# Performance work log

Measured on AMD Instinct MI355X. Metric: run time of the kernel, lower is better.

The kernel has to match this reference:

```python
import jax, jax.numpy as jnp
import numpy as np

D_STATE = 512
D_MODEL = 512
BATCH = 8
SEQ = 4096
DT_MIN, DT_MAX = 1e-3, 0.1
LN_EPS = 1e-5


def setup_inputs() -> dict:
    key = jax.random.key(0)
    ks = jax.random.split(key, 4)
    x = jax.random.normal(ks[0], (BATCH, SEQ, D_MODEL), dtype=jnp.float32)
    volatility_scale = jax.random.uniform(ks[1], (BATCH, SEQ, 1), dtype=jnp.float32)
    # parameters (mirroring the torch module's __init__)
    log_lambda_real = jnp.linspace(np.log(DT_MIN), np.log(DT_MAX), D_STATE).astype(jnp.float32)
    log_b = jax.random.uniform(ks[2], (D_STATE, 1), dtype=jnp.float32, minval=-0.5, maxval=0.5)
    c = jax.random.normal(ks[3], (1, D_STATE), dtype=jnp.float32) / np.sqrt(D_STATE)
    log_d = jnp.zeros((1,), jnp.float32)
    ts = np.array([1.0 / 24.0, 1.0, 5.0, 21.0, 63.0], np.float32)
    extra = np.linspace(63.0, 189.0, D_STATE - len(ts), dtype=np.float32)
    log_step = jnp.log(jnp.asarray(np.concatenate([ts, extra])))
    volatility_gate = jnp.ones((D_MODEL,), jnp.float32)
    alpha = jnp.asarray(0.7, jnp.float32)
    ln_weight = jnp.ones((D_STATE,), jnp.float32)
    ln_bias = jnp.zeros((D_STATE,), jnp.float32)
    return dict(x=x, volatility_scale=volatility_scale,
                log_lambda_real=log_lambda_real, log_b=log_b, c=c, log_d=log_d,
                log_step=log_step, volatility_gate=volatility_gate, alpha=alpha,
                ln_weight=ln_weight, ln_bias=ln_bias)


def reference(x, volatility_scale, log_lambda_real, log_b, c, log_d,
              log_step, volatility_gate, alpha, ln_weight, ln_bias):
    lam = -jnp.exp(log_lambda_real)              # [N], negative real poles
    step = jnp.exp(log_step)                     # [N], per-state timescale
    b = jnp.exp(log_b)[:, 0]                     # [N]
    d = jnp.exp(log_d)                           # [1], skip gain
    # bilinear (Tustin) discretization, paired per state
    z = step * lam                               # [N]
    a_disc = (2.0 + z) / (2.0 - z)               # [N]
    b_disc = step * (1.0 + a_disc) * b / 2.0     # [N]
    gate = jax.nn.sigmoid(volatility_gate)       # [D]
    c_vec = c[0]                                 # [N]

    def layer_norm(h):
        mu = jnp.mean(h, axis=-1, keepdims=True)
        var = jnp.var(h, axis=-1, keepdims=True)
        return (h - mu) * jax.lax.rsqrt(var + LN_EPS) * ln_weight + ln_bias

    def scan_step(h, inp):
        x_t, v_t = inp                           # [B,D], [B,1]
        h = a_disc * h + b_disc * x_t            # diagonal SSM update, [B,N]
        h = layer_norm(h)
        h = h / (1.0 + gate * v_t)               # volatility gating
        y_t = jnp.sum(h * c_vec, axis=-1, keepdims=True) + d * x_t  # [B,D]
        return h, y_t

    h0 = jnp.zeros((x.shape[0], a_disc.shape[0]), x.dtype)
    xs = (jnp.swapaxes(x, 0, 1), jnp.swapaxes(volatility_scale, 0, 1))  # time-major
    _, ys = jax.lax.scan(scan_step, h0, xs)      # [S,B,D]
    y = jnp.swapaxes(ys, 0, 1)                   # [B,S,D]
    al = jax.nn.sigmoid(alpha)
    return al * x + (1.0 - al) * y
```

## Files before the change

kernel.cpp:

```cpp
#include <hip/hip_runtime.h>
#include <cstdint>
#include <cstddef>

#define BATCH 8
#define SEQ   4096
#define DS    512
#define JPL   8
#define BLK   8
#define NBLK  (SEQ / BLK)

typedef float v2f __attribute__((ext_vector_type(2)));
typedef float v4f __attribute__((ext_vector_type(4)));

static __device__ __forceinline__ v2f lo2(v4f x) { return __builtin_shufflevector(x, x, 0, 1); }
static __device__ __forceinline__ v2f hi2(v4f x) { return __builtin_shufflevector(x, x, 2, 3); }

template <int CTRL>
__device__ __forceinline__ float dpp_add(float v) {
  int t = __builtin_amdgcn_update_dpp(0, __builtin_bit_cast(int, v), CTRL, 0xF, 0xF, true);
  return v + __builtin_bit_cast(float, t);
}
__device__ __forceinline__ float wave_sum64(float v) {
  v = dpp_add<0x111>(v);
  v = dpp_add<0x112>(v);
  v = dpp_add<0x114>(v);
  v = dpp_add<0x118>(v);
  v = dpp_add<0x142>(v);
  v = dpp_add<0x143>(v);
  return v;
}
__device__ __forceinline__ float bcast63(float v) {
  return __builtin_bit_cast(float, __builtin_amdgcn_readlane(__builtin_bit_cast(int, v), 63));
}

__device__ __forceinline__ void ld16(const float* g, float* l) {
  __builtin_amdgcn_global_load_lds(
      (const __attribute__((address_space(1))) void*)g,
      (__attribute__((address_space(3))) void*)l, 16, 0, 0);
}

__global__ __launch_bounds__(192, 1) void ssm_scan(
    const float* __restrict__ x, const float* __restrict__ vol,
    const float* __restrict__ llr, const float* __restrict__ logb,
    const float* __restrict__ cvec, const float* __restrict__ lstp,
    const float* __restrict__ vgat, const float* __restrict__ lnw,
    const float* __restrict__ lnb, float* __restrict__ sp)
{
  __shared__ float X0[4096], X1[4096];
  __shared__ float R0[4096], R1[4096];
  __shared__ float SC0[512], SC1[512];

  const int b    = blockIdx.x;
  const int lane = threadIdx.x & 63;
  const int wid  = threadIdx.x >> 6;

  if (wid == 1) {
    const float* xg = x + (size_t)b * SEQ * DS + lane * JPL;
    float* spb = sp + (size_t)b * SEQ;

    auto dma_blk = [&](int blk, float* Xs) {
#pragma unroll
      for (int u = 0; u < BLK; ++u) {
        const float* row = xg + (size_t)(blk * BLK + u) * DS;
        ld16(row,     Xs + u * 512);
        ld16(row + 4, Xs + u * 512 + 256);
      }
    };
    auto red_copy = [&](const float* SCs, int blk) {
      float s[BLK];
#pragma unroll
      for (int u = 0; u < BLK; ++u) s[u] = wave_sum64(SCs[u * 64 + lane]);
      if (lane == 63) {
#pragma unroll
        for (int u = 0; u < BLK; ++u) spb[blk * BLK + u] = s[u];
      }
    };

    dma_blk(0, X0);
    __syncthreads();
#pragma unroll 1
    for (int i2 = 0; i2 < NBLK; i2 += 2) {
      dma_blk(i2 + 1, X1);
      if (i2 > 0) red_copy(SC1, i2 - 1);
      __syncthreads();
      if (i2 + 2 < NBLK) dma_blk(i2 + 2, X0);
      red_copy(SC0, i2);
      __syncthreads();
    }
    red_copy(SC1, NBLK - 1);
  } else if (wid == 2) {
    v2f gate[4];
#pragma unroll
    for (int j = 0; j < JPL; ++j)
      gate[j >> 1][j & 1] = 1.0f / (1.0f + expf(-vgat[lane * JPL + j]));
    const float* vg = vol + (size_t)b * SEQ;

    auto rg_blk = [&](v4f Va, v4f Vb, float* Rs) {
#pragma unroll
      for (int u = 0; u < BLK; ++u) {
        float vt = (u < 4) ? Va[u] : Vb[u - 4];
        v4f r0, r1;
#pragma unroll
        for (int k = 0; k < 4; ++k) {
          v2f den = gate[k] * vt + 1.0f;
          float q0 = __builtin_amdgcn_rcpf(den.x);
          float q1 = __builtin_amdgcn_rcpf(den.y);
          if (k < 2) { r0[2 * k] = q0; r0[2 * k + 1] = q1; }
          else       { r1[2 * (k - 2)] = q0; r1[2 * (k - 2) + 1] = q1; }
        }
        *(v4f*)(Rs + u * 512 + lane * 4)       = r0;
        *(v4f*)(Rs + u * 512 + 256 + lane * 4) = r1;
      }
    };

    v4f V0a = *(const v4f*)(vg + 0), V0b = *(const v4f*)(vg + 4);
    v4f V1a = *(const v4f*)(vg + 8), V1b = *(const v4f*)(vg + 12);
    rg_blk(V0a, V0b, R0);
    __syncthreads();
#pragma unroll 1
    for (int i2 = 0; i2 < NBLK; i2 += 2) {
      if (i2 + 2 < NBLK) {
        V0a = *(const v4f*)(vg + (i2 + 2) * BLK);
        V0b = *(const v4f*)(vg + (i2 + 2) * BLK + 4);
      }
      rg_blk(V1a, V1b, R1);
      __syncthreads();
      if (i2 + 3 < NBLK) {
        V1a = *(const v4f*)(vg + (i2 + 3) * BLK);
        V1b = *(const v4f*)(vg + (i2 + 3) * BLK + 4);
      }
      if (i2 + 2 < NBLK) rg_blk(V0a, V0b, R0);
      __syncthreads();
    }
  } else {
    v2f a[4], bd[4], w[4], bias[4], cc[4];
#pragma unroll
    for (int j = 0; j < JPL; ++j) {
      int n = lane * JPL + j;
      float lam = -expf(llr[n]);
      float st  = expf(lstp[n]);
      float z   = st * lam;
      float ad  = (2.0f + z) / (2.0f - z);
      a[j >> 1][j & 1]    = ad;
      bd[j >> 1][j & 1]   = st * (1.0f + ad) * expf(logb[n]) * 0.5f;
      w[j >> 1][j & 1]    = lnw[n];
      bias[j >> 1][j & 1] = lnb[n];
      cc[j >> 1][j & 1]   = cvec[n];
    }
    v2f h[4];
#pragma unroll
    for (int k = 0; k < 4; ++k) h[k] = (v2f){0.0f, 0.0f};

    auto proc_blk = [&](const float* Xs, const float* Rs, float* SCs) {
#pragma unroll
      for (int u = 0; u < BLK; ++u) {
        v4f xx0 = *(const v4f*)(Xs + u * 512 + lane * 4);
        v4f xx1 = *(const v4f*)(Xs + u * 512 + 256 + lane * 4);
        v4f rr0 = *(const v4f*)(Rs + u * 512 + lane * 4);
        v4f rr1 = *(const v4f*)(Rs + u * 512 + 256 + lane * 4);
        v2f xs[4] = {lo2(xx0), hi2(xx0), lo2(xx1), hi2(xx1)};
        v2f rs[4] = {lo2(rr0), hi2(rr0), lo2(rr1), hi2(rr1)};

        v2f hr[4];
#pragma unroll
        for (int k = 0; k < 4; ++k)
          hr[k] = __builtin_elementwise_fma(a[k], h[k], bd[k] * xs[k]);

        v2f ts = (hr[0] + hr[1]) + (hr[2] + hr[3]);
        float s1 = ts.x + ts.y;
        v2f qs = (hr[0] * hr[0] + hr[1] * hr[1]) + (hr[2] * hr[2] + hr[3] * hr[3]);
        float s2 = qs.x + qs.y;

        s1 = bcast63(wave_sum64(s1));
        s2 = bcast63(wave_sum64(s2));
        float mu  = s1 * (1.0f / DS);
        float m2  = s2 * (1.0f / DS);
        float var = __builtin_fmaf(-mu, mu, m2);
        float inv = __builtin_amdgcn_rsqf(var + 1e-5f);

#pragma unroll
        for (int k = 0; k < 4; ++k) {
          v2f niw = w[k] * inv;
          v2f hb  = bias[k] - niw * mu;
          v2f hln = __builtin_elementwise_fma(hr[k], niw, hb);
          h[k] = hln * rs[k];
        }

        v2f d = h[0] * cc[0];
        d = __builtin_elementwise_fma(h[1], cc[1], d);
        d = __builtin_elementwise_fma(h[2], cc[2], d);
        d = __builtin_elementwise_fma(h[3], cc[3], d);
        SCs[u * 64 + lane] = d.x + d.y;
      }
    };

    __syncthreads();
#pragma unroll 1
    for (int i2 = 0; i2 < NBLK; i2 += 2) {
      proc_blk(X0, R0, SC0);
      __syncthreads();
      proc_blk(X1, R1, SC1);
      __syncthreads();
    }
  }
}

__global__ __launch_bounds__(256) void out_scalar(
    const float* __restrict__ x, const float* __restrict__ sp,
    const float* __restrict__ alpha_p, const float* __restrict__ logd_p,
    float* __restrict__ out)
{
  const int lane = threadIdx.x & 63;
  const size_t bt = (size_t)blockIdx.x * 4 + (threadIdx.x >> 6);

  float al   = 1.0f / (1.0f + expf(-alpha_p[0]));
  float dd   = expf(logd_p[0]);
  float coef = __builtin_fmaf(1.0f - al, dd, al);
  float c1   = 1.0f - al;

  float s = sp[bt] * c1;
  const v4f* x4 = (const v4f*)x;
  v4f* o4 = (v4f*)out;
  size_t base = bt * 128;
#pragma unroll
  for (int j = 0; j < 2; ++j) {
    size_t i = base + lane + (size_t)j * 64;
    v4f xv = x4[i];
    o4[i] = xv * coef + s;
  }
}

extern "C" void kernel_launch(void* const* d_in, const int* in_sizes, int n_in,
                              void* d_out, int out_size, void* d_ws, size_t ws_size,
                              hipStream_t stream) {
  const float* x    = (const float*)d_in[0];
  const float* vol  = (const float*)d_in[1];
  const float* llr  = (const float*)d_in[2];
  const float* logb = (const float*)d_in[3];
  const float* cvec = (const float*)d_in[4];
  const float* logd = (const float*)d_in[5];
  const float* lstp = (const float*)d_in[6];
  const float* vgat = (const float*)d_in[7];
  const float* alph = (const float*)d_in[8];
  const float* lnw  = (const float*)d_in[9];
  const float* lnb  = (const float*)d_in[10];
  float* sp   = (float*)d_ws;
  float* outf = (float*)d_out;

  ssm_scan<<<BATCH, 192, 0, stream>>>(x, vol, llr, logb, cvec, lstp,
                                      vgat, lnw, lnb, sp);
  out_scalar<<<BATCH * SEQ / 4, 256, 0, stream>>>(x, sp, alph, logd, outf);
}
```

Before: 694.8 us.

## Fuse output epilogue into scan kernel and algebraically shorten per-step recurrence

The separate output kernel is removed. The loader wave now computes the final blend from the x tile already held in LDS and writes the output directly, so x is no longer re-read from global memory. The compute wave's recurrence is also refactored algebraically: the decay factor is folded into the LN weight and bias, and the bias-times-c term is precomputed by the gate wave into a new LDS buffer. This shortens the serial dependency chain per timestep. The cost is extra work and global stores on the loader wave, which only runs on 8 blocks, so store bandwidth from so few CUs may limit throughput.

```diff
diff --git a/kernel.cpp b/kernel.cpp
--- a/kernel.cpp
+++ b/kernel.cpp
@@ -8,6 +8,7 @@
 #define JPL   8
 #define BLK   8
 #define NBLK  (SEQ / BLK)
+#define LN_EPS 1e-5f
 
 typedef float v2f __attribute__((ext_vector_type(2)));
 typedef float v4f __attribute__((ext_vector_type(4)));
@@ -44,11 +45,13 @@
     const float* __restrict__ llr, const float* __restrict__ logb,
     const float* __restrict__ cvec, const float* __restrict__ lstp,
     const float* __restrict__ vgat, const float* __restrict__ lnw,
-    const float* __restrict__ lnb, float* __restrict__ sp)
+    const float* __restrict__ lnb, const float* __restrict__ alph,
+    const float* __restrict__ logd, float* __restrict__ out)
 {
-  __shared__ float X0[4096], X1[4096];
-  __shared__ float R0[4096], R1[4096];
-  __shared__ float SC0[512], SC1[512];
+  __shared__ __attribute__((aligned(16))) float X0[4096], X1[4096];
+  __shared__ __attribute__((aligned(16))) float R0[4096], R1[4096];
+  __shared__ __attribute__((aligned(16))) float SC0[512], SC1[512];
+  __shared__ __attribute__((aligned(16))) float SB0[512], SB1[512];
 
   const int b    = blockIdx.x;
   const int lane = threadIdx.x & 63;
@@ -56,7 +59,11 @@
 
   if (wid == 1) {
     const float* xg = x + (size_t)b * SEQ * DS + lane * JPL;
-    float* spb = sp + (size_t)b * SEQ;
+    float* ob = out + (size_t)b * SEQ * DS;
+    float al   = 1.0f / (1.0f + expf(-alph[0]));
+    float dd   = expf(logd[0]);
+    float coef = __builtin_fmaf(1.0f - al, dd, al);
+    float c1   = 1.0f - al;
 
     auto dma_blk = [&](int blk, float* Xs) {
 #pragma unroll
@@ -66,13 +73,18 @@
         ld16(row + 4, Xs + u * 512 + 256);
       }
     };
-    auto red_copy = [&](const float* SCs, int blk) {
-      float s[BLK];
-#pragma unroll
-      for (int u = 0; u < BLK; ++u) s[u] = wave_sum64(SCs[u * 64 + lane]);
-      if (lane == 63) {
-#pragma unroll
-        for (int u = 0; u < BLK; ++u) spb[blk * BLK + u] = s[u];
+    auto out_blk = [&](const float* SCs, const float* Xs, int blk) {
+#pragma unroll
+      for (int u = 0; u < BLK; ++u) {
+        float s  = bcast63(wave_sum64(SCs[u * 64 + lane]));
+        float sc = c1 * s;
+        v4f xa = *(const v4f*)(Xs + u * 512 + lane * 4);
+        v4f xb = *(const v4f*)(Xs + u * 512 + 256 + lane * 4);
+        v4f ya = xa * coef + sc;
+        v4f yb = xb * coef + sc;
+        float* row = ob + (size_t)(blk * BLK + u) * DS + lane * 8;
+        *(v4f*)(row)     = ya;
+        *(v4f*)(row + 4) = yb;
       }
     };
 
@@ -80,22 +92,37 @@
     __syncthreads();
 #pragma unroll 1
     for (int i2 = 0; i2 < NBLK; i2 += 2) {
+      if (i2 > 0) {
+        out_blk(SC1, X1, i2 - 1);
+        asm volatile("s_waitcnt lgkmcnt(0)" ::: "memory");
+        __builtin_amdgcn_sched_barrier(0);
+      }
       dma_blk(i2 + 1, X1);
-      if (i2 > 0) red_copy(SC1, i2 - 1);
-      __syncthreads();
-      if (i2 + 2 < NBLK) dma_blk(i2 + 2, X0);
-      red_copy(SC0, i2);
-      __syncthreads();
-    }
-    red_copy(SC1, NBLK - 1);
+      __syncthreads();
+      out_blk(SC0, X0, i2);
+      if (i2 + 2 < NBLK) {
+        asm volatile("s_waitcnt lgkmcnt(0)" ::: "memory");
+        __builtin_amdgcn_sched_barrier(0);
+        dma_blk(i2 + 2, X0);
+      }
+      __syncthreads();
+    }
+    out_blk(SC1, X1, NBLK - 1);
   } else if (wid == 2) {
     v2f gate[4];
 #pragma unroll
     for (int j = 0; j < JPL; ++j)
       gate[j >> 1][j & 1] = 1.0f / (1.0f + expf(-vgat[lane * JPL + j]));
+    v4f cb0, cb1;
+#pragma unroll
+    for (int m = 0; m < 4; ++m) {
+      int n0 = lane * JPL + m, n1 = lane * JPL + 4 + m;
+      cb0[m] = cvec[n0] * lnb[n0];
+      cb1[m] = cvec[n1] * lnb[n1];
+    }
     const float* vg = vol + (size_t)b * SEQ;
 
-    auto rg_blk = [&](v4f Va, v4f Vb, float* Rs) {
+    auto rg_blk = [&](v4f Va, v4f Vb, float* Rs, float* SBs) {
 #pragma unroll
       for (int u = 0; u < BLK; ++u) {
         float vt = (u < 4) ? Va[u] : Vb[u - 4];
@@ -110,12 +137,16 @@
         }
         *(v4f*)(Rs + u * 512 + lane * 4)       = r0;
         *(v4f*)(Rs + u * 512 + 256 + lane * 4) = r1;
+        v4f md = cb0 * r0;
+        md = __builtin_elementwise_fma(cb1, r1, md);
+        v2f mh = lo2(md) + hi2(md);
+        SBs[u * 64 + lane] = mh.x + mh.y;
       }
     };
 
     v4f V0a = *(const v4f*)(vg + 0), V0b = *(const v4f*)(vg + 4);
     v4f V1a = *(const v4f*)(vg + 8), V1b = *(const v4f*)(vg + 12);
-    rg_blk(V0a, V0b, R0);
+    rg_blk(V0a, V0b, R0, SB0);
     __syncthreads();
 #pragma unroll 1
     for (int i2 = 0; i2 < NBLK; i2 += 2) {
@@ -123,17 +154,17 @@
         V0a = *(const v4f*)(vg + (i2 + 2) * BLK);
         V0b = *(const v4f*)(vg + (i2 + 2) * BLK + 4);
       }
-      rg_blk(V1a, V1b, R1);
+      rg_blk(V1a, V1b, R1, SB1);
       __syncthreads();
       if (i2 + 3 < NBLK) {
         V1a = *(const v4f*)(vg + (i2 + 3) * BLK);
         V1b = *(const v4f*)(vg + (i2 + 3) * BLK + 4);
       }
-      if (i2 + 2 < NBLK) rg_blk(V0a, V0b, R0);
+      if (i2 + 2 < NBLK) rg_blk(V0a, V0b, R0, SB0);
       __syncthreads();
     }
   } else {
-    v2f a[4], bd[4], w[4], bias[4], cc[4];
+    v2f bd[4], aw[4], ab[4], cw[4];
 #pragma unroll
     for (int j = 0; j < JPL; ++j) {
       int n = lane * JPL + j;
@@ -141,92 +172,80 @@
       float st  = expf(lstp[n]);
       float z   = st * lam;
       float ad  = (2.0f + z) / (2.0f - z);
-      a[j >> 1][j & 1]    = ad;
-      bd[j >> 1][j & 1]   = st * (1.0f + ad) * expf(logb[n]) * 0.5f;
-      w[j >> 1][j & 1]    = lnw[n];
-      bias[j >> 1][j & 1] = lnb[n];
-      cc[j >> 1][j & 1]   = cvec[n];
-    }
-    v2f h[4];
-#pragma unroll
-    for (int k = 0; k < 4; ++k) h[k] = (v2f){0.0f, 0.0f};
-
-    auto proc_blk = [&](const float* Xs, const float* Rs, float* SCs) {
+      float bdv = st * (1.0f + ad) * expf(logb[n]) * 0.5f;
+      float wv  = lnw[n], bi = lnb[n], cv = cvec[n];
+      bd[j >> 1][j & 1] = bdv;
+      aw[j >> 1][j & 1] = ad * wv;
+      ab[j >> 1][j & 1] = ad * bi;
+      cw[j >> 1][j & 1] = cv * wv;
+    }
+    v2f hp[4];
+#pragma unroll
+    for (int k = 0; k < 4; ++k) hp[k] = (v2f){0.0f, 0.0f};
+
+    auto proc_blk = [&](const float* Xs, const float* Rs, const float* SBs, float* SCs) {
 #pragma unroll
       for (int u = 0; u < BLK; ++u) {
         v4f xx0 = *(const v4f*)(Xs + u * 512 + lane * 4);
         v4f xx1 = *(const v4f*)(Xs + u * 512 + 256 + lane * 4);
         v4f rr0 = *(const v4f*)(Rs + u * 512 + lane * 4);
         v4f rr1 = *(const v4f*)(Rs + u * 512 + 256 + lane * 4);
+        float u3s = SBs[u * 64 + lane];
         v2f xs[4] = {lo2(xx0), hi2(xx0), lo2(xx1), hi2(xx1)};
         v2f rs[4] = {lo2(rr0), hi2(rr0), lo2(rr1), hi2(rr1)};
 
-        v2f hr[4];
-#pragma unroll
-        for (int k = 0; k < 4; ++k)
-          hr[k] = __builtin_elementwise_fma(a[k], h[k], bd[k] * xs[k]);
-
-        v2f ts = (hr[0] + hr[1]) + (hr[2] + hr[3]);
-        float s1 = ts.x + ts.y;
-        v2f qs = (hr[0] * hr[0] + hr[1] * hr[1]) + (hr[2] * hr[2] + hr[3] * hr[3]);
-        float s2 = qs.x + qs.y;
+        v2f hr[4], q[4], abrs[4];
+#pragma unroll
+        for (int k = 0; k < 4; ++k) {
+          hr[k]   = __builtin_elementwise_fma(bd[k], xs[k], hp[k]);
+          q[k]    = rs[k] * hr[k];
+          abrs[k] = ab[k] * rs[k];
+        }
+        v2f t01 = hr[0] + hr[1], t23 = hr[2] + hr[3];
+        v2f tt  = t01 + t23;
+        float s1 = tt.x + tt.y;
+        v2f m01 = hr[0] * hr[0];
+        m01 = __builtin_elementwise_fma(hr[1], hr[1], m01);
+        v2f m23 = hr[2] * hr[2];
+        m23 = __builtin_elementwise_fma(hr[3], hr[3], m23);
+        v2f mm = m01 + m23;
+        float s2 = mm.x + mm.y;
 
         s1 = bcast63(wave_sum64(s1));
         s2 = bcast63(wave_sum64(s2));
         float mu  = s1 * (1.0f / DS);
-        float m2  = s2 * (1.0f / DS);
-        float var = __builtin_fmaf(-mu, mu, m2);
-        float inv = __builtin_amdgcn_rsqf(var + 1e-5f);
-
+        float m2e = __builtin_fmaf(s2, 1.0f / DS, LN_EPS);
+        float var = __builtin_fmaf(-mu, mu, m2e);
+        float inv = __builtin_amdgcn_rsqf(var);
+
+        v2f muv = {mu, mu}, invv = {inv, inv};
+        v2f tv[4];
+#pragma unroll
+        for (int k = 0; k < 4; ++k)
+          tv[k] = __builtin_elementwise_fma(-muv, rs[k], q[k]);
 #pragma unroll
         for (int k = 0; k < 4; ++k) {
-          v2f niw = w[k] * inv;
-          v2f hb  = bias[k] - niw * mu;
-          v2f hln = __builtin_elementwise_fma(hr[k], niw, hb);
-          h[k] = hln * rs[k];
+          v2f sv = aw[k] * tv[k];
+          hp[k]  = __builtin_elementwise_fma(invv, sv, abrs[k]);
         }
-
-        v2f d = h[0] * cc[0];
-        d = __builtin_elementwise_fma(h[1], cc[1], d);
-        d = __builtin_elementwise_fma(h[2], cc[2], d);
-        d = __builtin_elementwise_fma(h[3], cc[3], d);
-        SCs[u * 64 + lane] = d.x + d.y;
+        v2f u0 = cw[0] * tv[0];
+        u0 = __builtin_elementwise_fma(cw[1], tv[1], u0);
+        v2f u2 = cw[2] * tv[2];
+        u2 = __builtin_elementwise_fma(cw[3], tv[3], u2);
+        v2f uu = u0 + u2;
+        float u1s = uu.x + uu.y;
+        SCs[u * 64 + lane] = __builtin_fmaf(inv, u1s, u3s);
       }
     };
 
     __syncthreads();
 #pragma unroll 1
     for (int i2 = 0; i2 < NBLK; i2 += 2) {
-      proc_blk(X0, R0, SC0);
-      __syncthreads();
-      proc_blk(X1, R1, SC1);
-      __syncthreads();
-    }
-  }
-}
-
-__global__ __launch_bounds__(256) void out_scalar(
-    const float* __restrict__ x, const float* __restrict__ sp,
-    const float* __restrict__ alpha_p, const float* __restrict__ logd_p,
-    float* __restrict__ out)
-{
-  const int lane = threadIdx.x & 63;
-  const size_t bt = (size_t)blockIdx.x * 4 + (threadIdx.x >> 6);
-
-  float al   = 1.0f / (1.0f + expf(-alpha_p[0]));
-  float dd   = expf(logd_p[0]);
-  float coef = __builtin_fmaf(1.0f - al, dd, al);
-  float c1   = 1.0f - al;
-
-  float s = sp[bt] * c1;
-  const v4f* x4 = (const v4f*)x;
-  v4f* o4 = (v4f*)out;
-  size_t base = bt * 128;
-#pragma unroll
-  for (int j = 0; j < 2; ++j) {
-    size_t i = base + lane + (size_t)j * 64;
-    v4f xv = x4[i];
-    o4[i] = xv * coef + s;
+      proc_blk(X0, R0, SB0, SC0);
+      __syncthreads();
+      proc_blk(X1, R1, SB1, SC1);
+      __syncthreads();
+    }
   }
 }
 
@@ -244,10 +263,8 @@
   const float* alph = (const float*)d_in[8];
   const float* lnw  = (const float*)d_in[9];
   const float* lnb  = (const float*)d_in[10];
-  float* sp   = (float*)d_ws;
   float* outf = (float*)d_out;
 
   ssm_scan<<<BATCH, 192, 0, stream>>>(x, vol, llr, logb, cvec, lstp,
-                                      vgat, lnw, lnb, sp);
-  out_scalar<<<BATCH * SEQ / 4, 256, 0, stream>>>(x, sp, alph, logd, outf);
-}
+                                      vgat, lnw, lnb, alph, logd, outf);
+}
```

Result: faster. 676.2 us (-2.7%).
